# Performance work log

Hardware: AMD Instinct MI355X
Metric: run time of the kernel (lower is better)

Reference implementation:

```python
import jax, jax.numpy as jnp
import numpy as np

C = 256
GROUPS = 32
HEADS = 4
EPS = 1e-5

def setup_inputs() -> dict:
    key = jax.random.key(0)
    ks = jax.random.split(key, 6)
    N, H, W = 4, 64, 64
    s = 1.0 / np.sqrt(C)
    return {
        "x": jax.random.normal(ks[0], (N, C, H, W), dtype=jnp.float32),
        "gamma": jnp.ones((C,), jnp.float32),
        "beta": jnp.zeros((C,), jnp.float32),
        "Wq": jax.random.normal(ks[1], (C, C), jnp.float32) * s,
        "Wk": jax.random.normal(ks[2], (C, C), jnp.float32) * s,
        "Wv": jax.random.normal(ks[3], (C, C), jnp.float32) * s,
        "Wp": jax.random.normal(ks[4], (C, C), jnp.float32) * s,
        "bp": jnp.zeros((C,), jnp.float32),
    }

def group_norm(x, gamma, beta):
    N, Cc, H, W = x.shape
    xg = x.reshape(N, GROUPS, Cc // GROUPS, H, W)
    mean = jnp.mean(xg, axis=(2, 3, 4), keepdims=True)
    var = jnp.var(xg, axis=(2, 3, 4), keepdims=True)
    xg = (xg - mean) * jax.lax.rsqrt(var + EPS)
    x = xg.reshape(N, Cc, H, W)
    return x * gamma[None, :, None, None] + beta[None, :, None, None]

def reference(x, gamma, beta, Wq, Wk, Wv, Wp, bp):
    N, Cc, H, W = x.shape
    dh = Cc // HEADS
    L = H * W
    xn = group_norm(x, gamma, beta)           # [N,C,H,W]
    xf = xn.reshape(N, Cc, L)                 # [N,C,L]
    # 1x1 convs == channel matmuls; split into heads: [N,heads,L,dh]
    def proj_heads(Wm):
        t = jnp.einsum('oc,ncl->nol', Wm, xf)
        return t.reshape(N, HEADS, dh, L).transpose(0, 1, 3, 2)
    q = proj_heads(Wq)
    k = proj_heads(Wk)
    v = proj_heads(Wv)
    scale = dh ** -0.5
    attn = jnp.einsum('nhld,nhmd->nhlm', q, k) * scale  # [N,heads,L,L]
    attn = jax.nn.softmax(attn, axis=-1)
    out = jnp.einsum('nhlm,nhmd->nhld', attn, v)        # [N,heads,L,dh]
    out = out.transpose(0, 1, 3, 2).reshape(N, Cc, L)   # [N,C,L]
    out = jnp.einsum('oc,ncl->nol', Wp, out) + bp[None, :, None]
    return out.reshape(N, Cc, H, W)
```

## Files before the change

### kernel.cpp

```cpp
#include <hip/hip_runtime.h>
#include <cstddef>
#include <cstdint>

#define NB 4
#define CC 256
#define LL 4096
#define NG 32
#define CPG 8
#define NH 4
#define DH 64
#define PSPLIT 4194304

static constexpr float EPSV  = 1e-5f;
static constexpr float SCALE_Q = 0.125f * 1.4426950408889634f;

typedef __attribute__((ext_vector_type(8))) short bf16x8;
typedef __attribute__((ext_vector_type(4))) float f32x4;
typedef _Float16 f16x8 __attribute__((ext_vector_type(8)));
typedef _Float16 f16x4 __attribute__((ext_vector_type(4)));
typedef __fp16  h16x2 __attribute__((ext_vector_type(2)));

__device__ __forceinline__ short f2bf(float f) {
  unsigned u = __float_as_uint(f);
  unsigned r = (u + 0x7fffu + ((u >> 16) & 1u)) >> 16;
  return (short)r;
}
__device__ __forceinline__ short f2h(float f) {
  union { _Float16 h; short s; } u;
  u.h = (_Float16)f;
  return u.s;
}
__device__ __forceinline__ int sw(int row, int chunk) {
  return row * 64 + ((chunk ^ (row & 7)) * 8);
}

__global__ __launch_bounds__(256) void wcvt_kernel(
    const float* __restrict__ Wq, const float* __restrict__ Wk,
    const float* __restrict__ Wv, const float* __restrict__ Wp,
    short* __restrict__ dst) {
  const int which = blockIdx.x >> 5;
  const float* src = (which == 0) ? Wq : (which == 1) ? Wk : (which == 2) ? Wv : Wp;
  const int base = (blockIdx.x & 31) * 2048 + threadIdx.x * 8;
  const float4 v0 = *(const float4*)(src + base);
  const float4 v1 = *(const float4*)(src + base + 4);
  short ob[8] __attribute__((aligned(16)));
  if (which < 3) {
    ob[0] = f2bf(v0.x); ob[1] = f2bf(v0.y); ob[2] = f2bf(v0.z); ob[3] = f2bf(v0.w);
    ob[4] = f2bf(v1.x); ob[5] = f2bf(v1.y); ob[6] = f2bf(v1.z); ob[7] = f2bf(v1.w);
  } else {
    ob[0] = f2h(v0.x); ob[1] = f2h(v0.y); ob[2] = f2h(v0.z); ob[3] = f2h(v0.w);
    ob[4] = f2h(v1.x); ob[5] = f2h(v1.y); ob[6] = f2h(v1.z); ob[7] = f2h(v1.w);
  }
  *(uint4*)(dst + which * 65536 + base) = *(const uint4*)ob;
}

__global__ __launch_bounds__(256) void gn_stats(
    const float* __restrict__ x, float* __restrict__ pstat) {
  const int blk = blockIdx.x;
  const int grp = blk >> 2, qtr = blk & 3;
  const float* xp = x + (size_t)grp * CPG * LL + qtr * 1024 + threadIdx.x * 4;

  float s = 0.f, ss = 0.f;
  #pragma unroll
  for (int cc = 0; cc < 8; ++cc) {
    const float4 v = *(const float4*)(xp + (size_t)cc * LL);
    s  += v.x + v.y + v.z + v.w;
    ss += v.x * v.x + v.y * v.y + v.z * v.z + v.w * v.w;
  }
  #pragma unroll
  for (int off = 32; off; off >>= 1) {
    s  += __shfl_down(s, off);
    ss += __shfl_down(ss, off);
  }
  __shared__ float r1[4], r2[4];
  const int wid = threadIdx.x >> 6, lane = threadIdx.x & 63;
  if (lane == 0) { r1[wid] = s; r2[wid] = ss; }
  __syncthreads();
  if (threadIdx.x == 0) {
    float S = 0.f, SS = 0.f;
    #pragma unroll
    for (int w = 0; w < 4; ++w) { S += r1[w]; SS += r2[w]; }
    pstat[blk * 2]     = S;
    pstat[blk * 2 + 1] = SS;
  }
}

__global__ __launch_bounds__(256) void gn_apply(
    const float* __restrict__ x, const float* __restrict__ gamma,
    const float* __restrict__ beta, const float* __restrict__ pstat,
    short* __restrict__ xnT) {
  const int blk = blockIdx.x;
  const int grp = blk >> 2, j = blk & 3;
  const int n = grp >> 5, g = grp & 31;
  const float* xp = x + (size_t)grp * CPG * LL;
  const int NE = CPG * LL;

  float S = 0.f, SS = 0.f;
  #pragma unroll
  for (int w = 0; w < 4; ++w) {
    S  += pstat[grp * 8 + w * 2];
    SS += pstat[grp * 8 + w * 2 + 1];
  }
  const float mean = S / NE;
  const float rstd = rsqrtf(SS / NE - mean * mean + EPSV);

  float scl[8], shf[8];
  #pragma unroll
  for (int cc = 0; cc < 8; ++cc) {
    const float gm = gamma[g * CPG + cc];
    scl[cc] = rstd * gm;
    shf[cc] = beta[g * CPG + cc] - mean * rstd * gm;
  }
  const int l = j * 1024 + threadIdx.x * 4;
  float4 vv[8];
  #pragma unroll
  for (int cc = 0; cc < 8; ++cc)
    vv[cc] = *(const float4*)(xp + (size_t)cc * LL + l);
  short ob[4][8] __attribute__((aligned(16)));
  #pragma unroll
  for (int cc = 0; cc < 8; ++cc) {
    ob[0][cc] = f2bf(vv[cc].x * scl[cc] + shf[cc]);
    ob[1][cc] = f2bf(vv[cc].y * scl[cc] + shf[cc]);
    ob[2][cc] = f2bf(vv[cc].z * scl[cc] + shf[cc]);
    ob[3][cc] = f2bf(vv[cc].w * scl[cc] + shf[cc]);
  }
  short* op = xnT + ((size_t)n * LL + l) * CC + g * CPG;
  #pragma unroll
  for (int ii = 0; ii < 4; ++ii)
    *(uint4*)(op + (size_t)ii * CC) = *(const uint4*)ob[ii];
}

__global__ __launch_bounds__(256) void qkv_gemm(
    const short* __restrict__ xnT, const short* __restrict__ Wqb,
    const short* __restrict__ Wkb, const short* __restrict__ Wvb,
    short* __restrict__ Qt, short* __restrict__ Kt, _Float16* __restrict__ Vo) {
  const int lt = blockIdx.x, ot = blockIdx.y;
  const int n = lt >> 6, l0 = (lt & 63) << 6;
  const int wave = threadIdx.x >> 6, lane = threadIdx.x & 63;
  const int lq = lane & 15, quad = lane >> 4;

  const int orow = ot * 64 + wave * 16 + lq;
  const short* wqp = Wqb + orow * CC + quad * 8;
  const short* wkp = Wkb + orow * CC + quad * 8;
  const short* wvp = Wvb + orow * CC + quad * 8;
  const short* xp  = xnT + ((size_t)(n * LL + l0) + lq) * CC + quad * 8;

  const f32x4 z = {0.f, 0.f, 0.f, 0.f};
  f32x4 aq[4] = {z, z, z, z}, ak[4] = {z, z, z, z}, av[4] = {z, z, z, z};

  #pragma unroll
  for (int c0 = 0; c0 < 256; c0 += 32) {
    const bf16x8 fq = *(const bf16x8*)(wqp + c0);
    const bf16x8 fk = *(const bf16x8*)(wkp + c0);
    const bf16x8 fv = *(const bf16x8*)(wvp + c0);
    #pragma unroll
    for (int n0 = 0; n0 < 4; ++n0) {
      const bf16x8 fb = *(const bf16x8*)(xp + (size_t)(n0 * 16) * CC + c0);
      aq[n0] = __builtin_amdgcn_mfma_f32_16x16x32_bf16(fq, fb, aq[n0], 0, 0, 0);
      ak[n0] = __builtin_amdgcn_mfma_f32_16x16x32_bf16(fk, fb, ak[n0], 0, 0, 0);
      av[n0] = __builtin_amdgcn_mfma_f32_16x16x32_bf16(fv, fb, av[n0], 0, 0, 0);
    }
  }

  const size_t hb = (size_t)(n * NH + ot);
  #pragma unroll
  for (int n0 = 0; n0 < 4; ++n0)
    #pragma unroll
    for (int r = 0; r < 4; ++r)
      Vo[(hb * DH + wave * 16 + quad * 4 + r) * LL + l0 + n0 * 16 + lq] =
          (_Float16)av[n0][r];
  __shared__ short qt_lds[64][72], kt_lds[64][72];
  #pragma unroll
  for (int n0 = 0; n0 < 4; ++n0)
    #pragma unroll
    for (int r = 0; r < 4; ++r) {
      qt_lds[n0 * 16 + lq][wave * 16 + quad * 4 + r] = f2bf(aq[n0][r] * SCALE_Q);
      kt_lds[n0 * 16 + lq][wave * 16 + quad * 4 + r] = f2bf(ak[n0][r]);
    }
  __syncthreads();
  #pragma unroll
  for (int i = 0; i < 2; ++i) {
    const int u = threadIdx.x + i * 256;
    const int row = u >> 3, ch = u & 7;
    *(uint4*)(Qt + (hb * LL + l0 + row) * DH + ch * 8) = *(const uint4*)&qt_lds[row][ch * 8];
    *(uint4*)(Kt + (hb * LL + l0 + row) * DH + ch * 8) = *(const uint4*)&kt_lds[row][ch * 8];
  }
}

__global__ __launch_bounds__(256, 2) void attn_mfma_kernel(
    const short* __restrict__ Qt, const short* __restrict__ Kt,
    const _Float16* __restrict__ Vb, _Float16* __restrict__ Opart,
    float* __restrict__ lpart) {
  __shared__ __align__(16) short    k_lds[2][64 * 64];
  __shared__ __align__(16) _Float16 v_lds[2][64 * 64];

  const int t = threadIdx.x;
  const int wave = t >> 6, lane = t & 63;
  const int lq = lane & 15, quad = lane >> 4;
  const int l0 = blockIdx.x * 256;
  const int h = blockIdx.y >> 1, split = blockIdx.y & 1;
  const int n = blockIdx.z;
  const int kbase = split * 2048;
  const int R = n * NH + h;
  const size_t hb = (size_t)R * (size_t)LL * DH;
  const short* const Kp = Kt + hb;
  const _Float16* const Vp = Vb + hb;

  const int qbase = l0 + wave * 64;
  bf16x8 qb[4][2];
  #pragma unroll
  for (int qf = 0; qf < 4; ++qf)
    #pragma unroll
    for (int c = 0; c < 2; ++c)
      qb[qf][c] = *(const bf16x8*)(Qt + hb + (size_t)(qbase + qf * 16 + lq) * DH + c * 32 + quad * 8);

  const f32x4 z = {0.f, 0.f, 0.f, 0.f};
  f32x4 o[4][4] = {{z, z, z, z}, {z, z, z, z}, {z, z, z, z}, {z, z, z, z}};
  f32x4 ol[4] = {z, z, z, z};

  f16x8 ones8;
  #pragma unroll
  for (int i = 0; i < 8; ++i) ones8[i] = (_Float16)1.0f;

  const int srow = t >> 3, sch = t & 7;
  const int vgo = 32 * (sch >> 2) + 4 * (sch & 3);

  {
    *(uint4*)&k_lds[0][sw(srow, sch)]      = *(const uint4*)(Kp + (size_t)(kbase + srow) * DH + sch * 8);
    *(uint4*)&k_lds[0][sw(32 + srow, sch)] = *(const uint4*)(Kp + (size_t)(kbase + 32 + srow) * DH + sch * 8);
    const _Float16* vg0 = Vp + (size_t)srow * LL + kbase + vgo;
    const _Float16* vg1 = Vp + (size_t)(32 + srow) * LL + kbase + vgo;
    uint2 a = *(const uint2*)vg0, b = *(const uint2*)(vg0 + 16);
    *(uint4*)&v_lds[0][sw(srow, sch)] = make_uint4(a.x, a.y, b.x, b.y);
    a = *(const uint2*)vg1; b = *(const uint2*)(vg1 + 16);
    *(uint4*)&v_lds[0][sw(32 + srow, sch)] = make_uint4(a.x, a.y, b.x, b.y);
  }
  __syncthreads();

  for (int kt = 0; kt < 32; ++kt) {
    const int cur = kt & 1;
    uint4 kpre[2]; uint2 vpre[4];
    if (kt < 31) {
      const int kpos = kbase + (kt + 1) * 64;
      kpre[0] = *(const uint4*)(Kp + (size_t)(kpos + srow) * DH + sch * 8);
      kpre[1] = *(const uint4*)(Kp + (size_t)(kpos + 32 + srow) * DH + sch * 8);
      const _Float16* vg0 = Vp + (size_t)srow * LL + kpos + vgo;
      const _Float16* vg1 = Vp + (size_t)(32 + srow) * LL + kpos + vgo;
      vpre[0] = *(const uint2*)vg0;
      vpre[1] = *(const uint2*)(vg0 + 16);
      vpre[2] = *(const uint2*)vg1;
      vpre[3] = *(const uint2*)(vg1 + 16);
    }
    const short* kb = k_lds[cur];
    const _Float16* vbuf = v_lds[cur];

    union PU { f16x4 h4[2]; f16x8 h8; } af[2][4];
    #pragma unroll
    for (int mf = 0; mf < 4; ++mf) {
      const bf16x8 ka0 = *(const bf16x8*)&kb[sw(mf * 16 + lq, quad)];
      const bf16x8 ka1 = *(const bf16x8*)&kb[sw(mf * 16 + lq, 4 + quad)];
      #pragma unroll
      for (int qf = 0; qf < 4; ++qf) {
        f32x4 zz = {0.f, 0.f, 0.f, 0.f};
        zz = __builtin_amdgcn_mfma_f32_16x16x32_bf16(ka0, qb[qf][0], zz, 0, 0, 0);
        zz = __builtin_amdgcn_mfma_f32_16x16x32_bf16(ka1, qb[qf][1], zz, 0, 0, 0);
        union { h16x2 h2[2]; f16x4 h4; } u;
        u.h2[0] = __builtin_amdgcn_cvt_pkrtz(__builtin_amdgcn_exp2f(zz[0]),
                                             __builtin_amdgcn_exp2f(zz[1]));
        u.h2[1] = __builtin_amdgcn_cvt_pkrtz(__builtin_amdgcn_exp2f(zz[2]),
                                             __builtin_amdgcn_exp2f(zz[3]));
        af[mf >> 1][qf].h4[mf & 1] = u.h4;
      }
    }

    #pragma unroll
    for (int qf = 0; qf < 4; ++qf) {
      ol[qf] = __builtin_amdgcn_mfma_f32_16x16x32_f16(af[0][qf].h8, ones8, ol[qf], 0, 0, 0);
      ol[qf] = __builtin_amdgcn_mfma_f32_16x16x32_f16(af[1][qf].h8, ones8, ol[qf], 0, 0, 0);
    }

    #pragma unroll
    for (int df = 0; df < 4; ++df)
      #pragma unroll
      for (int cc = 0; cc < 2; ++cc) {
        const f16x8 vb8 = *(const f16x8*)&vbuf[sw(df * 16 + lq, cc * 4 + quad)];
        #pragma unroll
        for (int qf = 0; qf < 4; ++qf)
          o[qf][df] = __builtin_amdgcn_mfma_f32_16x16x32_f16(af[cc][qf].h8, vb8, o[qf][df], 0, 0, 0);
      }

    if (kt < 31) {
      const int nxt = 1 - cur;
      *(uint4*)&k_lds[nxt][sw(srow, sch)]      = kpre[0];
      *(uint4*)&k_lds[nxt][sw(32 + srow, sch)] = kpre[1];
      *(uint4*)&v_lds[nxt][sw(srow, sch)]      = make_uint4(vpre[0].x, vpre[0].y, vpre[1].x, vpre[1].y);
      *(uint4*)&v_lds[nxt][sw(32 + srow, sch)] = make_uint4(vpre[2].x, vpre[2].y, vpre[3].x, vpre[3].y);
      __syncthreads();
    }
  }

  const size_t pb = ((size_t)split * 16 + R) * (size_t)LL * DH;
  #pragma unroll
  for (int qf = 0; qf < 4; ++qf) {
    if (lq == 0) {
      #pragma unroll
      for (int r = 0; r < 4; ++r)
        lpart[((size_t)split * 16 + R) * LL + qbase + qf * 16 + quad * 4 + r] = ol[qf][r];
    }
    #pragma unroll
    for (int df = 0; df < 4; ++df)
      #pragma unroll
      for (int r = 0; r < 4; ++r) {
        const int q = qbase + qf * 16 + quad * 4 + r;
        Opart[pb + (size_t)q * DH + df * 16 + lq] = (_Float16)o[qf][df][r];
      }
  }
}

__global__ __launch_bounds__(256) void proj_gemm(
    const _Float16* __restrict__ Opart, const float* __restrict__ lpart,
    const _Float16* __restrict__ Wpf, const float* __restrict__ bp,
    float* __restrict__ out) {
  const int lt = blockIdx.x, ot2 = blockIdx.y;
  const int n = lt >> 6, l0 = (lt & 63) << 6;
  const int wave = threadIdx.x >> 6, lane = threadIdx.x & 63;
  const int lq = lane & 15, quad = lane >> 4;

  const _Float16* wpp0 = Wpf + (ot2 * 128 + wave * 16 + lq) * CC + quad * 8;
  const _Float16* wpp1 = wpp0 + 64 * CC;

  _Float16 invl[4][4];
  #pragma unroll
  for (int n0 = 0; n0 < 4; ++n0) {
    const int q = l0 + n0 * 16 + lq;
    #pragma unroll
    for (int h = 0; h < 4; ++h) {
      const size_t rr = (size_t)(n * NH + h) * LL + q;
      invl[n0][h] = (_Float16)(1.0f / (lpart[rr] + lpart[rr + 16 * (size_t)LL]));
    }
  }

  const f32x4 z = {0.f, 0.f, 0.f, 0.f};
  f32x4 acc[2][4] = {{z, z, z, z}, {z, z, z, z}};
  #pragma unroll
  for (int c0 = 0; c0 < 256; c0 += 32) {
    const int h = c0 >> 6;
    const int d0 = (c0 & 63) + quad * 8;
    const f16x8 fa0 = *(const f16x8*)(wpp0 + c0);
    const f16x8 fa1 = *(const f16x8*)(wpp1 + c0);
    #pragma unroll
    for (int n0 = 0; n0 < 4; ++n0) {
      const int q = l0 + n0 * 16 + lq;
      const size_t e = ((size_t)(n * NH + h) * LL + q) * DH + d0;
      const f16x8 b0 = *(const f16x8*)(Opart + e);
      const f16x8 b1 = *(const f16x8*)(Opart + e + (size_t)PSPLIT);
      f16x8 sc8;
      #pragma unroll
      for (int i = 0; i < 8; ++i) sc8[i] = invl[n0][h];
      const f16x8 fb = (b0 + b1) * sc8;
      acc[0][n0] = __builtin_amdgcn_mfma_f32_16x16x32_f16(fa0, fb, acc[0][n0], 0, 0, 0);
      acc[1][n0] = __builtin_amdgcn_mfma_f32_16x16x32_f16(fa1, fb, acc[1][n0], 0, 0, 0);
    }
  }
  #pragma unroll
  for (int w = 0; w < 2; ++w)
    #pragma unroll
    for (int r = 0; r < 4; ++r) {
      const int oo = ot2 * 128 + w * 64 + wave * 16 + quad * 4 + r;
      const float bias = bp[oo];
      #pragma unroll
      for (int n0 = 0; n0 < 4; ++n0)
        out[((size_t)n * CC + oo) * LL + l0 + n0 * 16 + lq] = acc[w][n0][r] + bias;
    }
}

extern "C" void kernel_launch(void* const* d_in, const int* in_sizes, int n_in,
                              void* d_out, int out_size, void* d_ws, size_t ws_size,
                              hipStream_t stream) {
  const float* x     = (const float*)d_in[0];
  const float* gamma = (const float*)d_in[1];
  const float* beta  = (const float*)d_in[2];
  const float* Wq    = (const float*)d_in[3];
  const float* Wk    = (const float*)d_in[4];
  const float* Wv    = (const float*)d_in[5];
  const float* Wp    = (const float*)d_in[6];
  const float* bp    = (const float*)d_in[7];
  float* out = (float*)d_out;

  const size_t S = (size_t)NB * CC * LL;
  short*     xnT = (short*)d_ws;
  short*     Qt  = xnT + S;
  short*     Kt  = Qt + S;
  _Float16*  Vo  = (_Float16*)(Kt + S);
  short*     Wb  = (short*)(Vo + S);
  _Float16*  Opart = (_Float16*)(Wb + 4 * 65536);
  float*     lpart = (float*)(Opart + 2 * (size_t)PSPLIT);
  float*     pstat = lpart + 2 * 16 * (size_t)LL;

  gn_stats   <<<512,                  256, 0, stream>>>(x, pstat);
  gn_apply   <<<512,                  256, 0, stream>>>(x, gamma, beta, pstat, xnT);
  wcvt_kernel<<<128,                  256, 0, stream>>>(Wq, Wk, Wv, Wp, Wb);
  qkv_gemm   <<<dim3(256, 4),         256, 0, stream>>>(xnT, Wb, Wb + 65536, Wb + 131072, Qt, Kt, Vo);
  attn_mfma_kernel<<<dim3(LL/256, NH*2, NB), 256, 0, stream>>>(Qt, Kt, Vo, Opart, lpart);
  proj_gemm  <<<dim3(256, 2),         256, 0, stream>>>(Opart, lpart,
                 (const _Float16*)(Wb + 196608), bp, out);
}
```

Before: 205.4 us.

## Fuse GroupNorm apply into QKV GEMM and merge stats with weight conversion

Merges the group-norm statistics and weight-conversion kernels into a single launch, and moves the normalize-and-transpose step into the QKV GEMM. Each GEMM block now normalizes its 64-position tile of x straight into shared memory. This removes the xnT round trip through global memory and two kernel launches. In exchange, each block re-reads x and recomputes normalization redundantly across the 4 output tiles, and the GEMM now holds a larger shared-memory tile with an extra barrier.

```diff
diff --git a/kernel.cpp b/kernel.cpp
--- a/kernel.cpp
+++ b/kernel.cpp
@@ -34,116 +34,106 @@
   return row * 64 + ((chunk ^ (row & 7)) * 8);
 }
 
-__global__ __launch_bounds__(256) void wcvt_kernel(
+__global__ __launch_bounds__(256) void gnstats_wcvt(
+    const float* __restrict__ x, float* __restrict__ pstat,
     const float* __restrict__ Wq, const float* __restrict__ Wk,
     const float* __restrict__ Wv, const float* __restrict__ Wp,
-    short* __restrict__ dst) {
-  const int which = blockIdx.x >> 5;
-  const float* src = (which == 0) ? Wq : (which == 1) ? Wk : (which == 2) ? Wv : Wp;
-  const int base = (blockIdx.x & 31) * 2048 + threadIdx.x * 8;
-  const float4 v0 = *(const float4*)(src + base);
-  const float4 v1 = *(const float4*)(src + base + 4);
-  short ob[8] __attribute__((aligned(16)));
-  if (which < 3) {
-    ob[0] = f2bf(v0.x); ob[1] = f2bf(v0.y); ob[2] = f2bf(v0.z); ob[3] = f2bf(v0.w);
-    ob[4] = f2bf(v1.x); ob[5] = f2bf(v1.y); ob[6] = f2bf(v1.z); ob[7] = f2bf(v1.w);
+    short* __restrict__ wdst) {
+  __shared__ float r1[4], r2[4];
+  const int blk = blockIdx.x;
+  if (blk < 512) {
+    const int grp = blk >> 2, qtr = blk & 3;
+    const float* xp = x + (size_t)grp * CPG * LL + qtr * 1024 + threadIdx.x * 4;
+    float s = 0.f, ss = 0.f;
+    #pragma unroll
+    for (int cc = 0; cc < 8; ++cc) {
+      const float4 v = *(const float4*)(xp + (size_t)cc * LL);
+      s  += v.x + v.y + v.z + v.w;
+      ss += v.x * v.x + v.y * v.y + v.z * v.z + v.w * v.w;
+    }
+    #pragma unroll
+    for (int off = 32; off; off >>= 1) {
+      s  += __shfl_down(s, off);
+      ss += __shfl_down(ss, off);
+    }
+    const int wid = threadIdx.x >> 6, lane = threadIdx.x & 63;
+    if (lane == 0) { r1[wid] = s; r2[wid] = ss; }
+    __syncthreads();
+    if (threadIdx.x == 0) {
+      float S = 0.f, SS = 0.f;
+      #pragma unroll
+      for (int w = 0; w < 4; ++w) { S += r1[w]; SS += r2[w]; }
+      pstat[blk * 2]     = S;
+      pstat[blk * 2 + 1] = SS;
+    }
   } else {
-    ob[0] = f2h(v0.x); ob[1] = f2h(v0.y); ob[2] = f2h(v0.z); ob[3] = f2h(v0.w);
-    ob[4] = f2h(v1.x); ob[5] = f2h(v1.y); ob[6] = f2h(v1.z); ob[7] = f2h(v1.w);
-  }
-  *(uint4*)(dst + which * 65536 + base) = *(const uint4*)ob;
-}
-
-__global__ __launch_bounds__(256) void gn_stats(
-    const float* __restrict__ x, float* __restrict__ pstat) {
-  const int blk = blockIdx.x;
-  const int grp = blk >> 2, qtr = blk & 3;
-  const float* xp = x + (size_t)grp * CPG * LL + qtr * 1024 + threadIdx.x * 4;
-
-  float s = 0.f, ss = 0.f;
-  #pragma unroll
-  for (int cc = 0; cc < 8; ++cc) {
-    const float4 v = *(const float4*)(xp + (size_t)cc * LL);
-    s  += v.x + v.y + v.z + v.w;
-    ss += v.x * v.x + v.y * v.y + v.z * v.z + v.w * v.w;
-  }
-  #pragma unroll
-  for (int off = 32; off; off >>= 1) {
-    s  += __shfl_down(s, off);
-    ss += __shfl_down(ss, off);
-  }
-  __shared__ float r1[4], r2[4];
-  const int wid = threadIdx.x >> 6, lane = threadIdx.x & 63;
-  if (lane == 0) { r1[wid] = s; r2[wid] = ss; }
-  __syncthreads();
-  if (threadIdx.x == 0) {
-    float S = 0.f, SS = 0.f;
-    #pragma unroll
-    for (int w = 0; w < 4; ++w) { S += r1[w]; SS += r2[w]; }
-    pstat[blk * 2]     = S;
-    pstat[blk * 2 + 1] = SS;
-  }
-}
-
-__global__ __launch_bounds__(256) void gn_apply(
+    const int wblk = blk - 512;
+    const int which = wblk >> 5;
+    const float* src = (which == 0) ? Wq : (which == 1) ? Wk : (which == 2) ? Wv : Wp;
+    const int base = (wblk & 31) * 2048 + threadIdx.x * 8;
+    const float4 v0 = *(const float4*)(src + base);
+    const float4 v1 = *(const float4*)(src + base + 4);
+    short ob[8] __attribute__((aligned(16)));
+    if (which < 3) {
+      ob[0] = f2bf(v0.x); ob[1] = f2bf(v0.y); ob[2] = f2bf(v0.z); ob[3] = f2bf(v0.w);
+      ob[4] = f2bf(v1.x); ob[5] = f2bf(v1.y); ob[6] = f2bf(v1.z); ob[7] = f2bf(v1.w);
+    } else {
+      ob[0] = f2h(v0.x); ob[1] = f2h(v0.y); ob[2] = f2h(v0.z); ob[3] = f2h(v0.w);
+      ob[4] = f2h(v1.x); ob[5] = f2h(v1.y); ob[6] = f2h(v1.z); ob[7] = f2h(v1.w);
+    }
+    *(uint4*)(wdst + which * 65536 + base) = *(const uint4*)ob;
+  }
+}
+
+__global__ __launch_bounds__(256) void qkv_gemm(
     const float* __restrict__ x, const float* __restrict__ gamma,
     const float* __restrict__ beta, const float* __restrict__ pstat,
-    short* __restrict__ xnT) {
-  const int blk = blockIdx.x;
-  const int grp = blk >> 2, j = blk & 3;
-  const int n = grp >> 5, g = grp & 31;
-  const float* xp = x + (size_t)grp * CPG * LL;
-  const int NE = CPG * LL;
-
-  float S = 0.f, SS = 0.f;
-  #pragma unroll
-  for (int w = 0; w < 4; ++w) {
-    S  += pstat[grp * 8 + w * 2];
-    SS += pstat[grp * 8 + w * 2 + 1];
-  }
-  const float mean = S / NE;
-  const float rstd = rsqrtf(SS / NE - mean * mean + EPSV);
-
-  float scl[8], shf[8];
-  #pragma unroll
-  for (int cc = 0; cc < 8; ++cc) {
-    const float gm = gamma[g * CPG + cc];
-    scl[cc] = rstd * gm;
-    shf[cc] = beta[g * CPG + cc] - mean * rstd * gm;
-  }
-  const int l = j * 1024 + threadIdx.x * 4;
-  float4 vv[8];
-  #pragma unroll
-  for (int cc = 0; cc < 8; ++cc)
-    vv[cc] = *(const float4*)(xp + (size_t)cc * LL + l);
-  short ob[4][8] __attribute__((aligned(16)));
-  #pragma unroll
-  for (int cc = 0; cc < 8; ++cc) {
-    ob[0][cc] = f2bf(vv[cc].x * scl[cc] + shf[cc]);
-    ob[1][cc] = f2bf(vv[cc].y * scl[cc] + shf[cc]);
-    ob[2][cc] = f2bf(vv[cc].z * scl[cc] + shf[cc]);
-    ob[3][cc] = f2bf(vv[cc].w * scl[cc] + shf[cc]);
-  }
-  short* op = xnT + ((size_t)n * LL + l) * CC + g * CPG;
-  #pragma unroll
-  for (int ii = 0; ii < 4; ++ii)
-    *(uint4*)(op + (size_t)ii * CC) = *(const uint4*)ob[ii];
-}
-
-__global__ __launch_bounds__(256) void qkv_gemm(
-    const short* __restrict__ xnT, const short* __restrict__ Wqb,
-    const short* __restrict__ Wkb, const short* __restrict__ Wvb,
+    const short* __restrict__ Wqb, const short* __restrict__ Wkb,
+    const short* __restrict__ Wvb,
     short* __restrict__ Qt, short* __restrict__ Kt, _Float16* __restrict__ Vo) {
+  __shared__ __align__(16) short smem[64 * 264];
   const int lt = blockIdx.x, ot = blockIdx.y;
   const int n = lt >> 6, l0 = (lt & 63) << 6;
   const int wave = threadIdx.x >> 6, lane = threadIdx.x & 63;
   const int lq = lane & 15, quad = lane >> 4;
 
+  #pragma unroll
+  for (int i = 0; i < 2; ++i) {
+    const int u = threadIdx.x + i * 256;
+    const int cc = u >> 4, l4 = u & 15;
+    const int grp = n * NG + cc;
+    float S = 0.f, SS = 0.f;
+    #pragma unroll
+    for (int w = 0; w < 4; ++w) {
+      S  += pstat[(grp * 4 + w) * 2];
+      SS += pstat[(grp * 4 + w) * 2 + 1];
+    }
+    const float mean = S / 32768.f;
+    const float rstd = rsqrtf(SS / 32768.f - mean * mean + EPSV);
+    const float* xp = x + (size_t)(n * CC + cc * CPG) * LL + l0 + l4 * 4;
+    short ob[4][8] __attribute__((aligned(16)));
+    #pragma unroll
+    for (int j = 0; j < 8; ++j) {
+      const float scl = rstd * gamma[cc * CPG + j];
+      const float shf = beta[cc * CPG + j] - mean * scl;
+      const float4 v = *(const float4*)(xp + (size_t)j * LL);
+      ob[0][j] = f2bf(v.x * scl + shf);
+      ob[1][j] = f2bf(v.y * scl + shf);
+      ob[2][j] = f2bf(v.z * scl + shf);
+      ob[3][j] = f2bf(v.w * scl + shf);
+    }
+    short* dst = smem + (l4 * 4) * 264 + cc * 8;
+    #pragma unroll
+    for (int jj = 0; jj < 4; ++jj)
+      *(uint4*)(dst + jj * 264) = *(const uint4*)ob[jj];
+  }
+  __syncthreads();
+
   const int orow = ot * 64 + wave * 16 + lq;
   const short* wqp = Wqb + orow * CC + quad * 8;
   const short* wkp = Wkb + orow * CC + quad * 8;
   const short* wvp = Wvb + orow * CC + quad * 8;
-  const short* xp  = xnT + ((size_t)(n * LL + l0) + lq) * CC + quad * 8;
+  const short* xl  = smem + lq * 264 + quad * 8;
 
   const f32x4 z = {0.f, 0.f, 0.f, 0.f};
   f32x4 aq[4] = {z, z, z, z}, ak[4] = {z, z, z, z}, av[4] = {z, z, z, z};
@@ -155,7 +145,7 @@
     const bf16x8 fv = *(const bf16x8*)(wvp + c0);
     #pragma unroll
     for (int n0 = 0; n0 < 4; ++n0) {
-      const bf16x8 fb = *(const bf16x8*)(xp + (size_t)(n0 * 16) * CC + c0);
+      const bf16x8 fb = *(const bf16x8*)(xl + (n0 * 16) * 264 + c0);
       aq[n0] = __builtin_amdgcn_mfma_f32_16x16x32_bf16(fq, fb, aq[n0], 0, 0, 0);
       ak[n0] = __builtin_amdgcn_mfma_f32_16x16x32_bf16(fk, fb, ak[n0], 0, 0, 0);
       av[n0] = __builtin_amdgcn_mfma_f32_16x16x32_bf16(fv, fb, av[n0], 0, 0, 0);
@@ -169,21 +159,24 @@
     for (int r = 0; r < 4; ++r)
       Vo[(hb * DH + wave * 16 + quad * 4 + r) * LL + l0 + n0 * 16 + lq] =
           (_Float16)av[n0][r];
-  __shared__ short qt_lds[64][72], kt_lds[64][72];
+
+  __syncthreads();
+  short* qt_l = smem;
+  short* kt_l = smem + 64 * 72;
   #pragma unroll
   for (int n0 = 0; n0 < 4; ++n0)
     #pragma unroll
     for (int r = 0; r < 4; ++r) {
-      qt_lds[n0 * 16 + lq][wave * 16 + quad * 4 + r] = f2bf(aq[n0][r] * SCALE_Q);
-      kt_lds[n0 * 16 + lq][wave * 16 + quad * 4 + r] = f2bf(ak[n0][r]);
+      qt_l[(n0 * 16 + lq) * 72 + wave * 16 + quad * 4 + r] = f2bf(aq[n0][r] * SCALE_Q);
+      kt_l[(n0 * 16 + lq) * 72 + wave * 16 + quad * 4 + r] = f2bf(ak[n0][r]);
     }
   __syncthreads();
   #pragma unroll
   for (int i = 0; i < 2; ++i) {
     const int u = threadIdx.x + i * 256;
     const int row = u >> 3, ch = u & 7;
-    *(uint4*)(Qt + (hb * LL + l0 + row) * DH + ch * 8) = *(const uint4*)&qt_lds[row][ch * 8];
-    *(uint4*)(Kt + (hb * LL + l0 + row) * DH + ch * 8) = *(const uint4*)&kt_lds[row][ch * 8];
+    *(uint4*)(Qt + (hb * LL + l0 + row) * DH + ch * 8) = *(const uint4*)&qt_l[row * 72 + ch * 8];
+    *(uint4*)(Kt + (hb * LL + l0 + row) * DH + ch * 8) = *(const uint4*)&kt_l[row * 72 + ch * 8];
   }
 }
 
@@ -388,8 +381,7 @@
   float* out = (float*)d_out;
 
   const size_t S = (size_t)NB * CC * LL;
-  short*     xnT = (short*)d_ws;
-  short*     Qt  = xnT + S;
+  short*     Qt  = (short*)d_ws;
   short*     Kt  = Qt + S;
   _Float16*  Vo  = (_Float16*)(Kt + S);
   short*     Wb  = (short*)(Vo + S);
@@ -397,10 +389,9 @@
   float*     lpart = (float*)(Opart + 2 * (size_t)PSPLIT);
   float*     pstat = lpart + 2 * 16 * (size_t)LL;
 
-  gn_stats   <<<512,                  256, 0, stream>>>(x, pstat);
-  gn_apply   <<<512,                  256, 0, stream>>>(x, gamma, beta, pstat, xnT);
-  wcvt_kernel<<<128,                  256, 0, stream>>>(Wq, Wk, Wv, Wp, Wb);
-  qkv_gemm   <<<dim3(256, 4),         256, 0, stream>>>(xnT, Wb, Wb + 65536, Wb + 131072, Qt, Kt, Vo);
+  gnstats_wcvt<<<640,                 256, 0, stream>>>(x, pstat, Wq, Wk, Wv, Wp, Wb);
+  qkv_gemm   <<<dim3(256, 4),         256, 0, stream>>>(x, gamma, beta, pstat,
+                 Wb, Wb + 65536, Wb + 131072, Qt, Kt, Vo);
   attn_mfma_kernel<<<dim3(LL/256, NH*2, NB), 256, 0, stream>>>(Qt, Kt, Vo, Opart, lpart);
   proj_gemm  <<<dim3(256, 2),         256, 0, stream>>>(Opart, lpart,
                  (const _Float16*)(Wb + 196608), bp, out);
```

Measured after the change: 185.4 us. 9.7% less time.
